# Optimization experiments

Hardware: AMD Instinct MI355X
Metric: run time of the kernel (lower is better)

Reference implementation:

```python
import jax, jax.numpy as jnp
import numpy as np

V, D, S, B = 32000, 1024, 2048, 4
H = 4 * D


def _sinusoidal_pe(max_len, d):
    position = np.arange(max_len, dtype=np.float32)[:, None]
    div_term = np.exp(np.arange(0, d, 2, dtype=np.float32) * (-np.log(10000.0) / d))
    pe = np.zeros((max_len, d), dtype=np.float32)
    pe[:, 0::2] = np.sin(position * div_term)
    pe[:, 1::2] = np.cos(position * div_term)
    return jnp.asarray(pe)


def setup_inputs() -> dict:
    key = jax.random.key(0)
    ks = jax.random.split(key, 13)
    std = 1.0 / np.sqrt(D)
    stdh = 1.0 / np.sqrt(H)
    w = lambda k, shp, s: (jax.random.normal(k, shp, jnp.float32) * s)
    inp = {
        "tokens": jax.random.randint(ks[0], (B, S), 0, V),
        "emb": jax.random.normal(ks[1], (V, D), jnp.float32),
        "pe": _sinusoidal_pe(S, D),
        "l1_wk": w(ks[2], (D, D), std),
        "l1_wv": w(ks[3], (D, D), std),
        "l1_wo": w(ks[4], (D, D), std),
        "l1_w1": w(ks[5], (D, H), std),
        "l1_w2": w(ks[6], (H, D), stdh),
        "l2_wk": w(ks[7], (D, D), std),
        "l2_wv": w(ks[8], (D, D), std),
        "l2_wo": w(ks[9], (D, D), std),
        "l2_w1": w(ks[10], (D, H), std),
        "l2_w2": w(ks[11], (H, D), stdh),
        "w_out": w(ks[12], (D, V), std),
    }
    return inp


def _block(h, mask, wk, wv, wo, w1, w2):
    d = h.shape[-1]
    xq = h                      # W_q is identity
    xk = h @ wk                 # [B,S,D]
    xv = h @ wv
    scores = jnp.einsum("bsd,btd->bst", xq, xk) / np.sqrt(float(d)) + mask
    attn = jax.nn.softmax(scores, axis=-1)          # [B,S,S]
    h_attn = jnp.einsum("bst,btd->bsd", attn, xv) @ wo
    h_res = h + h_attn
    h_ffn = jnp.maximum(h_res @ w1, 0.0) @ w2
    return h_res + h_ffn


def reference(tokens, emb, pe, l1_wk, l1_wv, l1_wo, l1_w1, l1_w2,
              l2_wk, l2_wv, l2_wo, l2_w1, l2_w2, w_out):
    seq_len = tokens.shape[1]
    h = emb[tokens] + pe[None, :seq_len, :]
    # causal additive mask: -inf above diagonal
    mask = jnp.triu(jnp.full((seq_len, seq_len), -jnp.inf, jnp.float32), k=1)
    h = _block(h, mask, l1_wk, l1_wv, l1_wo, l1_w1, l1_w2)
    h = _block(h, mask, l2_wk, l2_wv, l2_wo, l2_w1, l2_w2)
    logits = h[:, -1, :] @ w_out  # [B, V]
    return logits
```

## Files before the change

### kernel.cpp

```cpp
#include <hip/hip_runtime.h>

#define S_LEN 2048
#define D_DIM 1024
#define H_DIM 4096
#define V_DIM 32000
#define B_SZ  4

typedef float  f32x4  __attribute__((ext_vector_type(4)));
typedef __bf16 bf16x8 __attribute__((ext_vector_type(8)));

__device__ __forceinline__ ushort f2bf(float f) {
    union { float f; unsigned u; } v; v.f = f;
    unsigned r = v.u + 0x7fffu + ((v.u >> 16) & 1u);
    return (ushort)(r >> 16);
}

__global__ void bt_wtranspose(const float* __restrict__ in, ushort* __restrict__ out,
                              int R, int C) {
    __shared__ ushort s[64][65];
    int r0 = blockIdx.y * 64, c0 = blockIdx.x * 64;
    int t = threadIdx.x;
    int lr = t >> 2, lc4 = (t & 3) * 16;
    const float* src = in + (size_t)(r0 + lr) * C + c0 + lc4;
#pragma unroll
    for (int j = 0; j < 4; ++j) {
        float4 v = ((const float4*)src)[j];
        s[lr][lc4 + 4 * j + 0] = f2bf(v.x);
        s[lr][lc4 + 4 * j + 1] = f2bf(v.y);
        s[lr][lc4 + 4 * j + 2] = f2bf(v.z);
        s[lr][lc4 + 4 * j + 3] = f2bf(v.w);
    }
    __syncthreads();
    int oc = t >> 2, orr = (t & 3) * 16;
    ushort tmp[16] __attribute__((aligned(16)));
#pragma unroll
    for (int j = 0; j < 16; ++j) tmp[j] = s[orr + j][oc];
    ushort* dst = out + (size_t)(c0 + oc) * R + r0 + orr;
    *(uint4*)dst        = *(uint4*)tmp;
    *(uint4*)(dst + 8)  = *(uint4*)(tmp + 8);
}

__global__ void bt_embed(const int* __restrict__ tokens, const float* __restrict__ emb,
                         const float* __restrict__ pe, float* __restrict__ h,
                         ushort* __restrict__ hbf) {
    int row = blockIdx.x;
    int s   = row & (S_LEN - 1);
    int tok = tokens[row];
    int t   = threadIdx.x;
    float4 v = ((const float4*)(emb + (size_t)tok * D_DIM))[t];
    float4 p = ((const float4*)(pe + (size_t)s * D_DIM))[t];
    v.x += p.x; v.y += p.y; v.z += p.z; v.w += p.w;
    ((float4*)(h + (size_t)row * D_DIM))[t] = v;
    uint2 pk;
    pk.x = (unsigned)f2bf(v.x) | ((unsigned)f2bf(v.y) << 16);
    pk.y = (unsigned)f2bf(v.z) | ((unsigned)f2bf(v.w) << 16);
    ((uint2*)(hbf + (size_t)row * D_DIM))[t] = pk;
}

#define EPI_F32  0
#define EPI_BF16 1
#define EPI_RELU 2
#define EPI_RES  3

template <int EPI, bool CSKIP, bool KLIM>
__global__ __launch_bounds__(256, 2)
void bt_gemm(const ushort* __restrict__ A, const ushort* __restrict__ B,
             float* __restrict__ Cf, ushort* __restrict__ Cb,
             const float* __restrict__ Res,
             int lda, int ldb, int ldc, int K,
             size_t strideA, size_t strideB, size_t strideC) {
    int bm = blockIdx.y, bn = blockIdx.x;
    if (CSKIP && bn > bm) return;

    __shared__ ushort sA[128 * 64];
    __shared__ ushort sB[128 * 64];

    const int tid  = threadIdx.x;
    const int lane = tid & 63;
    const int wv   = tid >> 6;
    const int wr   = wv >> 1, wc = wv & 1;
    const int r15  = lane & 15, r4 = lane >> 4;

    const ushort* Ab = A + strideA * blockIdx.z + (size_t)bm * 128 * lda;
    const ushort* Bb = B + strideB * blockIdx.z + (size_t)bn * 128 * ldb;

    int ktiles = K >> 6;
    if (KLIM) { int lim = (bm + 1) * 2; if (lim < ktiles) ktiles = lim; }

    f32x4 acc[4][4];
#pragma unroll
    for (int m = 0; m < 4; ++m)
#pragma unroll
        for (int n = 0; n < 4; ++n) acc[m][n] = (f32x4){0.f, 0.f, 0.f, 0.f};

    const int srow = wv * 8 + (lane >> 3);
    const int sout = lane & 7;

    for (int kt = 0; kt < ktiles; ++kt) {
        __syncthreads();
        const ushort* Ak = Ab + kt * 64;
        const ushort* Bk = Bb + kt * 64;
#pragma unroll
        for (int j = 0; j < 4; ++j) {
            int row = j * 32 + srow;
            int si  = sout ^ (row & 7);
            __builtin_amdgcn_global_load_lds(
                (const __attribute__((address_space(1))) void*)(Ak + (size_t)row * lda + si * 8),
                (__attribute__((address_space(3))) void*)(sA + j * 2048 + wv * 512), 16, 0, 0);
        }
#pragma unroll
        for (int j = 0; j < 4; ++j) {
            int row = j * 32 + srow;
            int si  = sout ^ (row & 7);
            __builtin_amdgcn_global_load_lds(
                (const __attribute__((address_space(1))) void*)(Bk + (size_t)row * ldb + si * 8),
                (__attribute__((address_space(3))) void*)(sB + j * 2048 + wv * 512), 16, 0, 0);
        }
        __syncthreads();
#pragma unroll
        for (int kk = 0; kk < 2; ++kk) {
            bf16x8 af[4], bv[4];
            int s = kk * 4 + r4;
#pragma unroll
            for (int m = 0; m < 4; ++m) {
                int row = wr * 64 + m * 16 + r15;
                af[m] = *(const bf16x8*)(sA + (size_t)row * 64 + (size_t)((s ^ (row & 7)) * 8));
            }
#pragma unroll
            for (int n = 0; n < 4; ++n) {
                int col = wc * 64 + n * 16 + r15;
                bv[n] = *(const bf16x8*)(sB + (size_t)col * 64 + (size_t)((s ^ (col & 7)) * 8));
            }
#pragma unroll
            for (int m = 0; m < 4; ++m)
#pragma unroll
                for (int n = 0; n < 4; ++n)
                    acc[m][n] = __builtin_amdgcn_mfma_f32_16x16x32_bf16(af[m], bv[n], acc[m][n], 0, 0, 0);
        }
    }

    size_t cz = strideC * blockIdx.z;
    int rowb = bm * 128 + wr * 64 + r4 * 4;
    int colb = bn * 128 + wc * 64 + r15;
#pragma unroll
    for (int m = 0; m < 4; ++m) {
#pragma unroll
        for (int r = 0; r < 4; ++r) {
            int row = rowb + m * 16 + r;
            size_t base = cz + (size_t)row * ldc + colb;
#pragma unroll
            for (int n = 0; n < 4; ++n) {
                float v = acc[m][n][r];
                size_t idx = base + n * 16;
                if (EPI == EPI_F32)       Cf[idx] = v;
                else if (EPI == EPI_BF16) Cb[idx] = f2bf(v);
                else if (EPI == EPI_RELU) Cb[idx] = f2bf(fmaxf(v, 0.f));
                else { float o = v + Res[idx]; Cf[idx] = o; Cb[idx] = f2bf(o); }
            }
        }
    }
}

__device__ __forceinline__ float wred_max(float v) {
#pragma unroll
    for (int off = 32; off; off >>= 1) v = fmaxf(v, __shfl_xor(v, off));
    return v;
}
__device__ __forceinline__ float wred_sum(float v) {
#pragma unroll
    for (int off = 32; off; off >>= 1) v += __shfl_xor(v, off);
    return v;
}

__global__ void bt_softmax(const float* __restrict__ scores, ushort* __restrict__ probs) {
    int row = blockIdx.x;
    int s   = row & (S_LEN - 1);
    const float* src = scores + (size_t)row * S_LEN;
    ushort*      dst = probs  + (size_t)row * S_LEN;
    int tid = threadIdx.x;
    int nvalid = s + 1;

    float vals[8];
    float mx = -1e30f;
#pragma unroll
    for (int j = 0; j < 8; ++j) {
        int t = tid + j * 256;
        float v = (t < nvalid) ? src[t] * 0.03125f : -1e30f;
        vals[j] = v;
        mx = fmaxf(mx, v);
    }
    __shared__ float red[4], red2[4];
    mx = wred_max(mx);
    if ((tid & 63) == 0) red[tid >> 6] = mx;
    __syncthreads();
    mx = fmaxf(fmaxf(red[0], red[1]), fmaxf(red[2], red[3]));

    float sum = 0.f, ps[8];
#pragma unroll
    for (int j = 0; j < 8; ++j) {
        float p = exp2f((vals[j] - mx) * 1.44269504f);
        ps[j] = p; sum += p;
    }
    sum = wred_sum(sum);
    if ((tid & 63) == 0) red2[tid >> 6] = sum;
    __syncthreads();
    sum = red2[0] + red2[1] + red2[2] + red2[3];
    float inv = 1.0f / sum;
#pragma unroll
    for (int j = 0; j < 8; ++j) {
        int t = tid + j * 256;
        dst[t] = (t < nvalid) ? f2bf(ps[j] * inv) : (ushort)0;
    }
}

__global__ void bt_logits(const float* __restrict__ h, const float* __restrict__ wout,
                          float* __restrict__ out) {
    __shared__ float hl[4][128];
    int tid = threadIdx.x;
    int d0 = blockIdx.y * 128;
    if (tid < 128) {
#pragma unroll
        for (int b = 0; b < 4; ++b)
            hl[b][tid] = h[((size_t)b * S_LEN + (S_LEN - 1)) * D_DIM + d0 + tid];
    }
    __syncthreads();
    int v = blockIdx.x * 256 + tid;
    float a0 = 0, a1 = 0, a2 = 0, a3 = 0;
    for (int j = 0; j < 128; ++j) {
        float w = wout[(size_t)(d0 + j) * V_DIM + v];
        a0 += hl[0][j] * w; a1 += hl[1][j] * w;
        a2 += hl[2][j] * w; a3 += hl[3][j] * w;
    }
    atomicAdd(out + v, a0);
    atomicAdd(out + V_DIM + v, a1);
    atomicAdd(out + 2 * V_DIM + v, a2);
    atomicAdd(out + 3 * V_DIM + v, a3);
}

extern "C" void kernel_launch(void* const* d_in, const int* in_sizes, int n_in,
                              void* d_out, int out_size, void* d_ws, size_t ws_size,
                              hipStream_t stream) {
    const int*   tokens = (const int*)d_in[0];
    const float* emb    = (const float*)d_in[1];
    const float* pe     = (const float*)d_in[2];
    const float* wgt[10];
    for (int i = 0; i < 10; ++i) wgt[i] = (const float*)d_in[3 + i];
    const float* wout = (const float*)d_in[13];

    char* w = (char*)d_ws;
    size_t o = 0;
    auto take = [&](size_t sz) { char* p = w + o; o += (sz + 255) & ~(size_t)255; return p; };

    const size_t DD = (size_t)D_DIM * D_DIM * 2;
    const size_t DH = (size_t)D_DIM * H_DIM * 2;
    size_t wsz[10] = {DD, DD, DD, DH, DH, DD, DD, DD, DH, DH};
    ushort* wT[10];
    for (int i = 0; i < 10; ++i) wT[i] = (ushort*)take(wsz[i]);

    const size_t NROW = (size_t)B_SZ * S_LEN;
    float*  h0     = (float*)take(NROW * D_DIM * 4);
    float*  h1     = (float*)take(NROW * D_DIM * 4);
    ushort* hbf    = (ushort*)take(NROW * D_DIM * 2);
    ushort* hresbf = (ushort*)take(NROW * D_DIM * 2);
    ushort* xkbf   = (ushort*)take(NROW * D_DIM * 2);
    ushort* xvt    = (ushort*)take((size_t)D_DIM * NROW * 2);
    ushort* hattn  = (ushort*)take(NROW * D_DIM * 2);
    char*   G      = take((size_t)B_SZ * S_LEN * S_LEN * 4 + (size_t)B_SZ * S_LEN * S_LEN * 2);
    float*  scores = (float*)G;
    ushort* probs  = (ushort*)(G + (size_t)B_SZ * S_LEN * S_LEN * 4);
    ushort* tbf    = (ushort*)G;

    int wR[10] = {1024, 1024, 1024, 1024, 4096, 1024, 1024, 1024, 1024, 4096};
    int wC[10] = {1024, 1024, 1024, 4096, 1024, 1024, 1024, 1024, 4096, 1024};
    for (int i = 0; i < 10; ++i)
        bt_wtranspose<<<dim3(wC[i] / 64, wR[i] / 64), 256, 0, stream>>>(wgt[i], wT[i], wR[i], wC[i]);

    bt_embed<<<NROW, 256, 0, stream>>>(tokens, emb, pe, h0, hbf);

    auto layer = [&](ushort* wk, ushort* wv2, ushort* wo, ushort* w1, ushort* w2) {
        bt_gemm<EPI_BF16, false, false><<<dim3(8, 64, 1), 256, 0, stream>>>(
            hbf, wk, nullptr, xkbf, nullptr, D_DIM, D_DIM, D_DIM, D_DIM, 0, 0, 0);
        bt_gemm<EPI_BF16, false, false><<<dim3(64, 8, 1), 256, 0, stream>>>(
            wv2, hbf, nullptr, xvt, nullptr, D_DIM, D_DIM, (int)NROW, D_DIM, 0, 0, 0);
        bt_gemm<EPI_F32, true, false><<<dim3(16, 16, B_SZ), 256, 0, stream>>>(
            hbf, xkbf, scores, nullptr, nullptr, D_DIM, D_DIM, S_LEN, D_DIM,
            (size_t)S_LEN * D_DIM, (size_t)S_LEN * D_DIM, (size_t)S_LEN * S_LEN);
        bt_softmax<<<NROW, 256, 0, stream>>>(scores, probs);
        bt_gemm<EPI_BF16, false, true><<<dim3(8, 16, B_SZ), 256, 0, stream>>>(
            probs, xvt, nullptr, hattn, nullptr, S_LEN, (int)NROW, D_DIM, S_LEN,
            (size_t)S_LEN * S_LEN, (size_t)S_LEN, (size_t)S_LEN * D_DIM);
        bt_gemm<EPI_RES, false, false><<<dim3(8, 64, 1), 256, 0, stream>>>(
            hattn, wo, h1, hresbf, h0, D_DIM, D_DIM, D_DIM, D_DIM, 0, 0, 0);
        bt_gemm<EPI_RELU, false, false><<<dim3(32, 64, 1), 256, 0, stream>>>(
            hresbf, w1, nullptr, tbf, nullptr, D_DIM, D_DIM, H_DIM, D_DIM, 0, 0, 0);
        bt_gemm<EPI_RES, false, false><<<dim3(8, 64, 1), 256, 0, stream>>>(
            tbf, w2, h0, hbf, h1, H_DIM, H_DIM, D_DIM, H_DIM, 0, 0, 0);
    };
    layer(wT[0], wT[1], wT[2], wT[3], wT[4]);
    layer(wT[5], wT[6], wT[7], wT[8], wT[9]);

    hipMemsetAsync(d_out, 0, (size_t)B_SZ * V_DIM * sizeof(float), stream);
    bt_logits<<<dim3(V_DIM / 256, D_DIM / 128), 256, 0, stream>>>(h0, wout, (float*)d_out);
}
```

Before: 873.8 us.

## Replace GEMM with 8-wave double-buffered kernel using larger tiles

Replaces the 256-thread 128x128 bf16 MFMA GEMM with a templated 512-thread kernel using 256x128 or 256x256 tiles. Global-to-LDS loads are double-buffered and split into K half-phases, so the next tile's loads overlap with the current MFMAs, with explicit vmcnt waits, barriers and raised wave priority during the MFMA blocks. The larger tiles are meant to cut global traffic per FLOP and hide load latency. In exchange there are fewer blocks per launch, one block per CU, and the causal skip and K-limit become coarser.

```diff
diff --git a/kernel.cpp b/kernel.cpp
--- a/kernel.cpp
+++ b/kernel.cpp
@@ -62,94 +62,120 @@
 #define EPI_RELU 2
 #define EPI_RES  3
 
-template <int EPI, bool CSKIP, bool KLIM>
-__global__ __launch_bounds__(256, 2)
-void bt_gemm(const ushort* __restrict__ A, const ushort* __restrict__ B,
-             float* __restrict__ Cf, ushort* __restrict__ Cb,
-             const float* __restrict__ Res,
-             int lda, int ldb, int ldc, int K,
-             size_t strideA, size_t strideB, size_t strideC) {
-    int bm = blockIdx.y, bn = blockIdx.x;
-    if (CSKIP && bn > bm) return;
-
-    __shared__ ushort sA[128 * 64];
-    __shared__ ushort sB[128 * 64];
+#define VMWAIT(N) asm volatile("s_waitcnt vmcnt(%0)" :: "n"(N) : "memory")
+#define SBAR()  __builtin_amdgcn_s_barrier()
+#define SCHED() __builtin_amdgcn_sched_barrier(0)
+#define AS1 __attribute__((address_space(1)))
+#define AS3 __attribute__((address_space(3)))
+
+template <int BM, int BN, int EPI, bool CSKIP, bool KLIM>
+__global__ __launch_bounds__(512, 1)
+void bt_gemm8(const ushort* __restrict__ A, const ushort* __restrict__ B,
+              float* Cf, ushort* Cb, const float* __restrict__ Res,
+              int lda, int ldb, int ldc, int K,
+              size_t strideA, size_t strideB, size_t strideC) {
+    constexpr int MR = BM / 32;
+    constexpr int NR = BN / 64;
+    constexpr int Ak = BM / 128;
+    constexpr int Bk = BN / 128;
+
+    __shared__ ushort lds[2][(BM + BN) * 64];
+
+    const int bm = blockIdx.y, bn = blockIdx.x;
+    if (CSKIP && bn * BN >= (bm + 1) * BM) return;
 
     const int tid  = threadIdx.x;
     const int lane = tid & 63;
-    const int wv   = tid >> 6;
-    const int wr   = wv >> 1, wc = wv & 1;
+    const int wid  = tid >> 6;
+    const int wr   = wid >> 2, wc = wid & 3;
     const int r15  = lane & 15, r4 = lane >> 4;
-
-    const ushort* Ab = A + strideA * blockIdx.z + (size_t)bm * 128 * lda;
-    const ushort* Bb = B + strideB * blockIdx.z + (size_t)bn * 128 * ldb;
-
-    int ktiles = K >> 6;
-    if (KLIM) { int lim = (bm + 1) * 2; if (lim < ktiles) ktiles = lim; }
-
-    f32x4 acc[4][4];
-#pragma unroll
-    for (int m = 0; m < 4; ++m)
-#pragma unroll
-        for (int n = 0; n < 4; ++n) acc[m][n] = (f32x4){0.f, 0.f, 0.f, 0.f};
-
-    const int srow = wv * 8 + (lane >> 3);
-    const int sout = lane & 7;
-
-    for (int kt = 0; kt < ktiles; ++kt) {
-        __syncthreads();
-        const ushort* Ak = Ab + kt * 64;
-        const ushort* Bk = Bb + kt * 64;
-#pragma unroll
-        for (int j = 0; j < 4; ++j) {
-            int row = j * 32 + srow;
-            int si  = sout ^ (row & 7);
-            __builtin_amdgcn_global_load_lds(
-                (const __attribute__((address_space(1))) void*)(Ak + (size_t)row * lda + si * 8),
-                (__attribute__((address_space(3))) void*)(sA + j * 2048 + wv * 512), 16, 0, 0);
-        }
-#pragma unroll
-        for (int j = 0; j < 4; ++j) {
-            int row = j * 32 + srow;
-            int si  = sout ^ (row & 7);
-            __builtin_amdgcn_global_load_lds(
-                (const __attribute__((address_space(1))) void*)(Bk + (size_t)row * ldb + si * 8),
-                (__attribute__((address_space(3))) void*)(sB + j * 2048 + wv * 512), 16, 0, 0);
-        }
-        __syncthreads();
-#pragma unroll
-        for (int kk = 0; kk < 2; ++kk) {
-            bf16x8 af[4], bv[4];
-            int s = kk * 4 + r4;
-#pragma unroll
-            for (int m = 0; m < 4; ++m) {
-                int row = wr * 64 + m * 16 + r15;
-                af[m] = *(const bf16x8*)(sA + (size_t)row * 64 + (size_t)((s ^ (row & 7)) * 8));
-            }
-#pragma unroll
-            for (int n = 0; n < 4; ++n) {
-                int col = wc * 64 + n * 16 + r15;
-                bv[n] = *(const bf16x8*)(sB + (size_t)col * 64 + (size_t)((s ^ (col & 7)) * 8));
-            }
-#pragma unroll
-            for (int m = 0; m < 4; ++m)
-#pragma unroll
-                for (int n = 0; n < 4; ++n)
-                    acc[m][n] = __builtin_amdgcn_mfma_f32_16x16x32_bf16(af[m], bv[n], acc[m][n], 0, 0, 0);
-        }
-    }
+    const int lr   = lane >> 2;
+    const int lsl  = lane & 3;
+    const int kswz = (r4 ^ ((r15 >> 1) & 3)) * 8;
+
+    const ushort* Ab = A + strideA * blockIdx.z + (size_t)bm * BM * lda;
+    const ushort* Bb = B + strideB * blockIdx.z + (size_t)bn * BN * ldb;
+
+    int NT = K >> 6;
+    if (KLIM) { int lim = (bm + 1) * (BM / 64); if (lim < NT) NT = lim; }
+
+    f32x4 acc[MR][NR];
+#pragma unroll
+    for (int m = 0; m < MR; ++m)
+#pragma unroll
+        for (int n = 0; n < NR; ++n) acc[m][n] = (f32x4){0.f, 0.f, 0.f, 0.f};
+
+#define STAGE(t, kh)                                                              \
+    {                                                                             \
+        _Pragma("unroll")                                                         \
+        for (int j = 0; j < Ak; ++j) {                                            \
+            int row = (wid + j * 8) * 16 + lr;                                    \
+            int c   = (kh) * 4 + (lsl ^ ((lr >> 1) & 3));                         \
+            __builtin_amdgcn_global_load_lds(                                     \
+                (const AS1 void*)(Ab + (size_t)(t) * 64 + (size_t)row * lda + c * 8), \
+                (AS3 void*)(&lds[(t) & 1][(kh) * BM * 32] + (wid + j * 8) * 512), 16, 0, 0); \
+        }                                                                         \
+        _Pragma("unroll")                                                         \
+        for (int j = 0; j < Bk; ++j) {                                            \
+            int row = (wid + j * 8) * 16 + lr;                                    \
+            int c   = (kh) * 4 + (lsl ^ ((lr >> 1) & 3));                         \
+            __builtin_amdgcn_global_load_lds(                                     \
+                (const AS1 void*)(Bb + (size_t)(t) * 64 + (size_t)row * ldb + c * 8), \
+                (AS3 void*)(&lds[(t) & 1][BM * 64 + (kh) * BN * 32] + (wid + j * 8) * 512), 16, 0, 0); \
+        }                                                                         \
+    }
+
+#define PHASE_COMPUTE(t, kh)                                                      \
+    {                                                                             \
+        bf16x8 aq[MR], bq[NR];                                                    \
+        _Pragma("unroll")                                                         \
+        for (int m = 0; m < MR; ++m) {                                            \
+            int row = wr * (BM / 2) + m * 16 + r15;                               \
+            aq[m] = *(const bf16x8*)(&lds[(t) & 1][(kh) * BM * 32 + row * 32 + kswz]); \
+        }                                                                         \
+        _Pragma("unroll")                                                         \
+        for (int n = 0; n < NR; ++n) {                                            \
+            int col = wc * (BN / 4) + n * 16 + r15;                               \
+            bq[n] = *(const bf16x8*)(&lds[(t) & 1][BM * 64 + (kh) * BN * 32 + col * 32 + kswz]); \
+        }                                                                         \
+        __builtin_amdgcn_s_setprio(1);                                            \
+        _Pragma("unroll")                                                         \
+        for (int m = 0; m < MR; ++m)                                              \
+            _Pragma("unroll")                                                     \
+            for (int n = 0; n < NR; ++n)                                          \
+                acc[m][n] = __builtin_amdgcn_mfma_f32_16x16x32_bf16(aq[m], bq[n], acc[m][n], 0, 0, 0); \
+        __builtin_amdgcn_s_setprio(0);                                            \
+    }
+
+    STAGE(0, 0); STAGE(0, 1);
+
+    for (int t = 0; t < NT - 1; ++t) {
+        VMWAIT(Ak + Bk); SBAR(); SCHED();
+        STAGE(t + 1, 0);
+        PHASE_COMPUTE(t, 0);
+        SCHED();
+        VMWAIT(Ak + Bk); SBAR(); SCHED();
+        STAGE(t + 1, 1);
+        PHASE_COMPUTE(t, 1);
+        SCHED();
+    }
+    VMWAIT(Ak + Bk); SBAR(); SCHED();
+    PHASE_COMPUTE(NT - 1, 0);
+    SCHED();
+    VMWAIT(0); SBAR(); SCHED();
+    PHASE_COMPUTE(NT - 1, 1);
 
     size_t cz = strideC * blockIdx.z;
-    int rowb = bm * 128 + wr * 64 + r4 * 4;
-    int colb = bn * 128 + wc * 64 + r15;
-#pragma unroll
-    for (int m = 0; m < 4; ++m) {
+    const int rowb = bm * BM + wr * (BM / 2) + r4 * 4;
+    const int colb = bn * BN + wc * (BN / 4) + r15;
+#pragma unroll
+    for (int m = 0; m < MR; ++m) {
 #pragma unroll
         for (int r = 0; r < 4; ++r) {
             int row = rowb + m * 16 + r;
             size_t base = cz + (size_t)row * ldc + colb;
 #pragma unroll
-            for (int n = 0; n < 4; ++n) {
+            for (int n = 0; n < NR; ++n) {
                 float v = acc[m][n][r];
                 size_t idx = base + n * 16;
                 if (EPI == EPI_F32)       Cf[idx] = v;
@@ -159,6 +185,8 @@
             }
         }
     }
+#undef STAGE
+#undef PHASE_COMPUTE
 }
 
 __device__ __forceinline__ float wred_max(float v) {
@@ -278,22 +306,22 @@
     bt_embed<<<NROW, 256, 0, stream>>>(tokens, emb, pe, h0, hbf);
 
     auto layer = [&](ushort* wk, ushort* wv2, ushort* wo, ushort* w1, ushort* w2) {
-        bt_gemm<EPI_BF16, false, false><<<dim3(8, 64, 1), 256, 0, stream>>>(
+        bt_gemm8<256, 128, EPI_BF16, false, false><<<dim3(8, 32, 1), 512, 0, stream>>>(
             hbf, wk, nullptr, xkbf, nullptr, D_DIM, D_DIM, D_DIM, D_DIM, 0, 0, 0);
-        bt_gemm<EPI_BF16, false, false><<<dim3(64, 8, 1), 256, 0, stream>>>(
+        bt_gemm8<128, 256, EPI_BF16, false, false><<<dim3(32, 8, 1), 512, 0, stream>>>(
             wv2, hbf, nullptr, xvt, nullptr, D_DIM, D_DIM, (int)NROW, D_DIM, 0, 0, 0);
-        bt_gemm<EPI_F32, true, false><<<dim3(16, 16, B_SZ), 256, 0, stream>>>(
+        bt_gemm8<256, 128, EPI_F32, true, false><<<dim3(16, 8, B_SZ), 512, 0, stream>>>(
             hbf, xkbf, scores, nullptr, nullptr, D_DIM, D_DIM, S_LEN, D_DIM,
             (size_t)S_LEN * D_DIM, (size_t)S_LEN * D_DIM, (size_t)S_LEN * S_LEN);
         bt_softmax<<<NROW, 256, 0, stream>>>(scores, probs);
-        bt_gemm<EPI_BF16, false, true><<<dim3(8, 16, B_SZ), 256, 0, stream>>>(
+        bt_gemm8<256, 128, EPI_BF16, false, true><<<dim3(8, 8, B_SZ), 512, 0, stream>>>(
             probs, xvt, nullptr, hattn, nullptr, S_LEN, (int)NROW, D_DIM, S_LEN,
             (size_t)S_LEN * S_LEN, (size_t)S_LEN, (size_t)S_LEN * D_DIM);
-        bt_gemm<EPI_RES, false, false><<<dim3(8, 64, 1), 256, 0, stream>>>(
+        bt_gemm8<256, 128, EPI_RES, false, false><<<dim3(8, 32, 1), 512, 0, stream>>>(
             hattn, wo, h1, hresbf, h0, D_DIM, D_DIM, D_DIM, D_DIM, 0, 0, 0);
-        bt_gemm<EPI_RELU, false, false><<<dim3(32, 64, 1), 256, 0, stream>>>(
+        bt_gemm8<256, 256, EPI_RELU, false, false><<<dim3(16, 32, 1), 512, 0, stream>>>(
             hresbf, w1, nullptr, tbf, nullptr, D_DIM, D_DIM, H_DIM, D_DIM, 0, 0, 0);
-        bt_gemm<EPI_RES, false, false><<<dim3(8, 64, 1), 256, 0, stream>>>(
+        bt_gemm8<256, 128, EPI_RES, false, false><<<dim3(8, 32, 1), 512, 0, stream>>>(
             tbf, w2, h0, hbf, h1, H_DIM, H_DIM, D_DIM, H_DIM, 0, 0, 0);
     };
     layer(wT[0], wT[1], wT[2], wT[3], wT[4]);
```

New measurement: 913.8 us. 1.05x slower.

## Fuse K/V projections into one GEMM and add XCD-aware block swizzle

Applied to the files above, without the earlier changes.

The K and V projection weights are packed side by side so a single GEMM produces both xk and xv into an interleaved buffer. A separate bf16 transpose kernel then builds the V-transposed operand that the PV GEMM needs, replacing the old dedicated transposed V GEMM. A new swizzle template maps linear block IDs so each of the 8 XCDs works on a contiguous band of row tiles, aiming to improve L2 reuse for the dense weight GEMMs. The cost is an extra transpose pass over V, and the swizzle assumes the grid's y dimension divides by 8.

```diff
diff --git a/kernel.cpp b/kernel.cpp
--- a/kernel.cpp
+++ b/kernel.cpp
@@ -38,6 +38,29 @@
     ushort* dst = out + (size_t)(c0 + oc) * R + r0 + orr;
     *(uint4*)dst        = *(uint4*)tmp;
     *(uint4*)(dst + 8)  = *(uint4*)(tmp + 8);
+}
+
+__global__ void bt_transpose(const ushort* __restrict__ in, ushort* __restrict__ out,
+                             int R, int ldin, int coff) {
+    __shared__ ushort s[64][65];
+    int r0 = blockIdx.y * 64, c0 = blockIdx.x * 64;
+    int t = threadIdx.x;
+    int lr = t >> 2, lc = (t & 3) * 16;
+    const ushort* src = in + (size_t)(r0 + lr) * ldin + coff + c0 + lc;
+    uint4 v0 = ((const uint4*)src)[0];
+    uint4 v1 = ((const uint4*)src)[1];
+    ushort tin[16] __attribute__((aligned(16)));
+    *(uint4*)tin = v0; *(uint4*)(tin + 8) = v1;
+#pragma unroll
+    for (int j = 0; j < 16; ++j) s[lr][lc + j] = tin[j];
+    __syncthreads();
+    int oc = t >> 2, orr = (t & 3) * 16;
+    ushort tmp[16] __attribute__((aligned(16)));
+#pragma unroll
+    for (int j = 0; j < 16; ++j) tmp[j] = s[orr + j][oc];
+    ushort* dst = out + (size_t)(c0 + oc) * R + r0 + orr;
+    *(uint4*)dst       = *(uint4*)tmp;
+    *(uint4*)(dst + 8) = *(uint4*)(tmp + 8);
 }
 
 __global__ void bt_embed(const int* __restrict__ tokens, const float* __restrict__ emb,
@@ -62,18 +85,29 @@
 #define EPI_RELU 2
 #define EPI_RES  3
 
-template <int EPI, bool CSKIP, bool KLIM>
+#define AS1 __attribute__((address_space(1)))
+#define AS3 __attribute__((address_space(3)))
+
+template <int EPI, bool CSKIP, bool KLIM, int SWZ>
 __global__ __launch_bounds__(256, 2)
 void bt_gemm(const ushort* __restrict__ A, const ushort* __restrict__ B,
-             float* __restrict__ Cf, ushort* __restrict__ Cb,
-             const float* __restrict__ Res,
+             float* Cf, ushort* Cb, const float* __restrict__ Res,
              int lda, int ldb, int ldc, int K,
              size_t strideA, size_t strideB, size_t strideC) {
-    int bm = blockIdx.y, bn = blockIdx.x;
-    if (CSKIP && bn > bm) return;
-
     __shared__ ushort sA[128 * 64];
     __shared__ ushort sB[128 * 64];
+
+    int bm, bn;
+    if (SWZ == 1) {
+        int gx = gridDim.x, gy = gridDim.y;
+        int id = blockIdx.y * gx + blockIdx.x;
+        int xcd = id & 7, slot = id >> 3;
+        int bandH = gy >> 3;
+        bm = xcd * bandH + (slot % bandH);
+        bn = slot / bandH;
+    } else { bm = blockIdx.y; bn = blockIdx.x; }
+
+    if (CSKIP && bn > bm) return;
 
     const int tid  = threadIdx.x;
     const int lane = tid & 63;
@@ -105,16 +139,16 @@
             int row = j * 32 + srow;
             int si  = sout ^ (row & 7);
             __builtin_amdgcn_global_load_lds(
-                (const __attribute__((address_space(1))) void*)(Ak + (size_t)row * lda + si * 8),
-                (__attribute__((address_space(3))) void*)(sA + j * 2048 + wv * 512), 16, 0, 0);
+                (const AS1 void*)(Ak + (size_t)row * lda + si * 8),
+                (AS3 void*)(sA + j * 2048 + wv * 512), 16, 0, 0);
         }
 #pragma unroll
         for (int j = 0; j < 4; ++j) {
             int row = j * 32 + srow;
             int si  = sout ^ (row & 7);
             __builtin_amdgcn_global_load_lds(
-                (const __attribute__((address_space(1))) void*)(Bk + (size_t)row * ldb + si * 8),
-                (__attribute__((address_space(3))) void*)(sB + j * 2048 + wv * 512), 16, 0, 0);
+                (const AS1 void*)(Bk + (size_t)row * ldb + si * 8),
+                (AS3 void*)(sB + j * 2048 + wv * 512), 16, 0, 0);
         }
         __syncthreads();
 #pragma unroll
@@ -140,8 +174,8 @@
     }
 
     size_t cz = strideC * blockIdx.z;
-    int rowb = bm * 128 + wr * 64 + r4 * 4;
-    int colb = bn * 128 + wc * 64 + r15;
+    const int rowb = bm * 128 + wr * 64 + r4 * 4;
+    const int colb = bn * 128 + wc * 64 + r15;
 #pragma unroll
     for (int m = 0; m < 4; ++m) {
 #pragma unroll
@@ -243,8 +277,6 @@
     const int*   tokens = (const int*)d_in[0];
     const float* emb    = (const float*)d_in[1];
     const float* pe     = (const float*)d_in[2];
-    const float* wgt[10];
-    for (int i = 0; i < 10; ++i) wgt[i] = (const float*)d_in[3 + i];
     const float* wout = (const float*)d_in[13];
 
     char* w = (char*)d_ws;
@@ -253,16 +285,21 @@
 
     const size_t DD = (size_t)D_DIM * D_DIM * 2;
     const size_t DH = (size_t)D_DIM * H_DIM * 2;
-    size_t wsz[10] = {DD, DD, DD, DH, DH, DD, DD, DD, DH, DH};
-    ushort* wT[10];
-    for (int i = 0; i < 10; ++i) wT[i] = (ushort*)take(wsz[i]);
-
     const size_t NROW = (size_t)B_SZ * S_LEN;
+
+    ushort* wkvT[2]; ushort* woT[2]; ushort* w1T[2]; ushort* w2T[2];
+    for (int l = 0; l < 2; ++l) {
+        wkvT[l] = (ushort*)take(2 * DD);
+        woT[l]  = (ushort*)take(DD);
+        w1T[l]  = (ushort*)take(DH);
+        w2T[l]  = (ushort*)take(DH);
+    }
+
     float*  h0     = (float*)take(NROW * D_DIM * 4);
     float*  h1     = (float*)take(NROW * D_DIM * 4);
     ushort* hbf    = (ushort*)take(NROW * D_DIM * 2);
     ushort* hresbf = (ushort*)take(NROW * D_DIM * 2);
-    ushort* xkbf   = (ushort*)take(NROW * D_DIM * 2);
+    ushort* xkv    = (ushort*)take(NROW * 2 * D_DIM * 2);
     ushort* xvt    = (ushort*)take((size_t)D_DIM * NROW * 2);
     ushort* hattn  = (ushort*)take(NROW * D_DIM * 2);
     char*   G      = take((size_t)B_SZ * S_LEN * S_LEN * 4 + (size_t)B_SZ * S_LEN * S_LEN * 2);
@@ -270,34 +307,41 @@
     ushort* probs  = (ushort*)(G + (size_t)B_SZ * S_LEN * S_LEN * 4);
     ushort* tbf    = (ushort*)G;
 
-    int wR[10] = {1024, 1024, 1024, 1024, 4096, 1024, 1024, 1024, 1024, 4096};
-    int wC[10] = {1024, 1024, 1024, 4096, 1024, 1024, 1024, 1024, 4096, 1024};
-    for (int i = 0; i < 10; ++i)
-        bt_wtranspose<<<dim3(wC[i] / 64, wR[i] / 64), 256, 0, stream>>>(wgt[i], wT[i], wR[i], wC[i]);
+    for (int l = 0; l < 2; ++l) {
+        const float* wk = (const float*)d_in[3 + 5 * l + 0];
+        const float* wv = (const float*)d_in[3 + 5 * l + 1];
+        const float* wo = (const float*)d_in[3 + 5 * l + 2];
+        const float* w1 = (const float*)d_in[3 + 5 * l + 3];
+        const float* w2 = (const float*)d_in[3 + 5 * l + 4];
+        bt_wtranspose<<<dim3(16, 16), 256, 0, stream>>>(wk, wkvT[l], 1024, 1024);
+        bt_wtranspose<<<dim3(16, 16), 256, 0, stream>>>(wv, wkvT[l] + (size_t)D_DIM * D_DIM, 1024, 1024);
+        bt_wtranspose<<<dim3(16, 16), 256, 0, stream>>>(wo, woT[l], 1024, 1024);
+        bt_wtranspose<<<dim3(64, 16), 256, 0, stream>>>(w1, w1T[l], 1024, 4096);
+        bt_wtranspose<<<dim3(16, 64), 256, 0, stream>>>(w2, w2T[l], 4096, 1024);
+    }
 
     bt_embed<<<NROW, 256, 0, stream>>>(tokens, emb, pe, h0, hbf);
 
-    auto layer = [&](ushort* wk, ushort* wv2, ushort* wo, ushort* w1, ushort* w2) {
-        bt_gemm<EPI_BF16, false, false><<<dim3(8, 64, 1), 256, 0, stream>>>(
-            hbf, wk, nullptr, xkbf, nullptr, D_DIM, D_DIM, D_DIM, D_DIM, 0, 0, 0);
-        bt_gemm<EPI_BF16, false, false><<<dim3(64, 8, 1), 256, 0, stream>>>(
-            wv2, hbf, nullptr, xvt, nullptr, D_DIM, D_DIM, (int)NROW, D_DIM, 0, 0, 0);
-        bt_gemm<EPI_F32, true, false><<<dim3(16, 16, B_SZ), 256, 0, stream>>>(
-            hbf, xkbf, scores, nullptr, nullptr, D_DIM, D_DIM, S_LEN, D_DIM,
-            (size_t)S_LEN * D_DIM, (size_t)S_LEN * D_DIM, (size_t)S_LEN * S_LEN);
+    auto layer = [&](int l) {
+        bt_gemm<EPI_BF16, false, false, 1><<<dim3(16, 64), 256, 0, stream>>>(
+            hbf, wkvT[l], nullptr, xkv, nullptr, D_DIM, D_DIM, 2 * D_DIM, D_DIM, 0, 0, 0);
+        bt_transpose<<<dim3(16, 128), 256, 0, stream>>>(xkv, xvt, (int)NROW, 2 * D_DIM, D_DIM);
+        bt_gemm<EPI_F32, true, false, 0><<<dim3(16, 16, B_SZ), 256, 0, stream>>>(
+            hbf, xkv, scores, nullptr, nullptr, D_DIM, 2 * D_DIM, S_LEN, D_DIM,
+            (size_t)S_LEN * D_DIM, (size_t)S_LEN * 2 * D_DIM, (size_t)S_LEN * S_LEN);
         bt_softmax<<<NROW, 256, 0, stream>>>(scores, probs);
-        bt_gemm<EPI_BF16, false, true><<<dim3(8, 16, B_SZ), 256, 0, stream>>>(
+        bt_gemm<EPI_BF16, false, true, 0><<<dim3(8, 16, B_SZ), 256, 0, stream>>>(
             probs, xvt, nullptr, hattn, nullptr, S_LEN, (int)NROW, D_DIM, S_LEN,
             (size_t)S_LEN * S_LEN, (size_t)S_LEN, (size_t)S_LEN * D_DIM);
-        bt_gemm<EPI_RES, false, false><<<dim3(8, 64, 1), 256, 0, stream>>>(
-            hattn, wo, h1, hresbf, h0, D_DIM, D_DIM, D_DIM, D_DIM, 0, 0, 0);
-        bt_gemm<EPI_RELU, false, false><<<dim3(32, 64, 1), 256, 0, stream>>>(
-            hresbf, w1, nullptr, tbf, nullptr, D_DIM, D_DIM, H_DIM, D_DIM, 0, 0, 0);
-        bt_gemm<EPI_RES, false, false><<<dim3(8, 64, 1), 256, 0, stream>>>(
-            tbf, w2, h0, hbf, h1, H_DIM, H_DIM, D_DIM, H_DIM, 0, 0, 0);
+        bt_gemm<EPI_RES, false, false, 1><<<dim3(8, 64), 256, 0, stream>>>(
+            hattn, woT[l], h1, hresbf, h0, D_DIM, D_DIM, D_DIM, D_DIM, 0, 0, 0);
+        bt_gemm<EPI_RELU, false, false, 1><<<dim3(32, 64), 256, 0, stream>>>(
+            hresbf, w1T[l], nullptr, tbf, nullptr, D_DIM, D_DIM, H_DIM, D_DIM, 0, 0, 0);
+        bt_gemm<EPI_RES, false, false, 1><<<dim3(8, 64), 256, 0, stream>>>(
+            tbf, w2T[l], h0, hbf, h1, H_DIM, H_DIM, D_DIM, H_DIM, 0, 0, 0);
     };
-    layer(wT[0], wT[1], wT[2], wT[3], wT[4]);
-    layer(wT[5], wT[6], wT[7], wT[8], wT[9]);
+    layer(0);
+    layer(1);
 
     hipMemsetAsync(d_out, 0, (size_t)B_SZ * V_DIM * sizeof(float), stream);
     bt_logits<<<dim3(V_DIM / 256, D_DIM / 128), 256, 0, stream>>>(h0, wout, (float*)d_out);
```

Measured after the change: 894.0 us. 1.02x slower.
